# Optimization experiments

Hardware: AMD Instinct MI355X
Metric: run time of the kernel (lower is better)

The kernel has to match this reference:

```python
import jax, jax.numpy as jnp
import numpy as np

N, E, D, H, HEADS_C, G = 50000, 800000, 128, 4, 32, 8
EDIM = D + 2  # H_update: phys_term (D) + ortho_geom (2)


def setup_inputs() -> dict:
    key = jax.random.key(0)
    ks = jax.random.split(key, 24)
    def gl(k, shape, fan_in):
        return jax.random.normal(k, shape, jnp.float32) / np.sqrt(fan_in)
    inp = {
        'h_target': jax.random.normal(ks[0], (N, D), jnp.float32),
        'h_source': jax.random.normal(ks[1], (N, D), jnp.float32),
        'edge_index': jax.random.randint(ks[2], (2, E), 0, N, jnp.int64),
        'pos': jax.random.uniform(ks[3], (N, 2), jnp.float32),
        't_emb': jax.random.normal(ks[4], (1, D), jnp.float32),
        # AdaGN params
        'gn_w': jnp.ones((D,), jnp.float32),
        'gn_b': jnp.zeros((D,), jnp.float32),
        'fc_W': gl(ks[5], (D, 2 * D), D),
        'fc_b': jnp.zeros((2 * D,), jnp.float32),
        # GATv2 params (lin_l, lin_r, lin_edge, att, bias)
        'Wl': gl(ks[6], (D, D), D),
        'bl': jnp.zeros((D,), jnp.float32),
        'Wr': gl(ks[7], (D, D), D),
        'br': jnp.zeros((D,), jnp.float32),
        'We': gl(ks[8], (EDIM, D), EDIM),
        'att': gl(ks[9], (H, HEADS_C), HEADS_C),
        'gat_b': jnp.zeros((D,), jnp.float32),
        # post_gat
        'Wp': gl(ks[10], (D, D), D),
        'bp': jnp.zeros((D,), jnp.float32),
        # update_mlp: LayerNorm + Linear(D,2D) + GELU + Linear(2D,D)
        'ln_w': jnp.ones((D,), jnp.float32),
        'ln_b': jnp.zeros((D,), jnp.float32),
        'W1': gl(ks[11], (D, 2 * D), D),
        'b1': jnp.zeros((2 * D,), jnp.float32),
        'W2': gl(ks[12], (2 * D, D), 2 * D),
        'b2': jnp.zeros((D,), jnp.float32),
    }
    return inp


def _adagn(x, cond, gn_w, gn_b, fc_W, fc_b):
    n, d = x.shape
    xg = x.reshape(n, G, d // G)
    mu = xg.mean(-1, keepdims=True)
    var = xg.var(-1, keepdims=True)  # biased, as torch GroupNorm
    normed = ((xg - mu) / jnp.sqrt(var + 1e-5)).reshape(n, d) * gn_w + gn_b
    style = cond @ fc_W + fc_b  # (1, 2D) broadcasts over nodes
    gamma, beta = jnp.split(style, 2, axis=-1)
    return normed * (1 + gamma) + beta


def _gatv2(h, edge_attr, src, dst, Wl, bl, Wr, br, We, att, gat_b):
    n = h.shape[0]
    x_l = (h @ Wl + bl).reshape(n, H, HEADS_C)  # source transform
    x_r = (h @ Wr + br).reshape(n, H, HEADS_C)  # target transform
    e_feat = (edge_attr @ We).reshape(-1, H, HEADS_C)
    x = x_l[src] + x_r[dst] + e_feat            # (E, H, C)
    x = jax.nn.leaky_relu(x, 0.2)
    logit = jnp.einsum('ehc,hc->eh', x, att)    # (E, H)
    # segment softmax over edges grouped by destination node
    amax = jax.ops.segment_max(logit, dst, num_segments=n)
    amax = jnp.where(jnp.isfinite(amax), amax, 0.0)
    ex = jnp.exp(logit - amax[dst])
    denom = jax.ops.segment_sum(ex, dst, num_segments=n)
    alpha = ex / (denom[dst] + 1e-16)           # (E, H)
    msg = x_l[src] * alpha[:, :, None]          # (E, H, C)
    out = jax.ops.segment_sum(msg, dst, num_segments=n)  # (N, H, C)
    return out.reshape(n, H * HEADS_C) + gat_b


def reference(h_target, h_source, edge_index, pos, t_emb,
              gn_w, gn_b, fc_W, fc_b,
              Wl, bl, Wr, br, We, att, gat_b,
              Wp, bp, ln_w, ln_b, W1, b1, W2, b2):
    h_mod = _adagn(h_source, t_emb, gn_w, gn_b, fc_W, fc_b)
    src, dst = edge_index[0], edge_index[1]
    rel_pos = pos[src] - pos[dst]                       # (E, 2)
    dist_sq = (rel_pos ** 2).sum(-1, keepdims=True) + 1e-8
    geom = rel_pos / dist_sq
    phys = h_mod[src] - h_mod[dst]                      # H_update mode
    ortho = jnp.stack([-geom[:, 1], geom[:, 0]], axis=-1)
    edge_attr = jnp.concatenate([phys, ortho], axis=-1)  # (E, D+2)
    aggr = _gatv2(h_mod, edge_attr, src, dst, Wl, bl, Wr, br, We, att, gat_b)
    aggr = aggr @ Wp + bp
    # update_mlp (dropout inactive in eval)
    mu = aggr.mean(-1, keepdims=True)
    var = aggr.var(-1, keepdims=True)
    z = (aggr - mu) / jnp.sqrt(var + 1e-5) * ln_w + ln_b
    z = jax.nn.gelu(z @ W1 + b1, approximate=False)
    delta = z @ W2 + b2
    return h_target + delta
```

## Files before the change

kernel.cpp:

```cpp
#include <hip/hip_runtime.h>
#include <math.h>

#define D 128
#define LOG2E 1.44269504088896340736f

typedef short bf16x4 __attribute__((ext_vector_type(4)));
typedef short bf16x8 __attribute__((ext_vector_type(8)));
typedef float f32x4  __attribute__((ext_vector_type(4)));
typedef float f32x2  __attribute__((ext_vector_type(2)));

__device__ __forceinline__ float b2f(unsigned short u) {
  union { unsigned int i; float f; } v; v.i = ((unsigned int)u) << 16; return v.f;
}
__device__ __forceinline__ unsigned short f2b(float f) {
  union { float f; unsigned int i; } v; v.f = f;
  unsigned int i = v.i;
  return (unsigned short)((i + 0x7FFFu + ((i >> 16) & 1u)) >> 16);
}
__device__ __forceinline__ float b2f_lo(unsigned int u) {
  union { unsigned int i; float f; } v; v.i = u << 16; return v.f;
}
__device__ __forceinline__ float b2f_hi(unsigned int u) {
  union { unsigned int i; float f; } v; v.i = u & 0xFFFF0000u; return v.f;
}
__device__ __forceinline__ float loadf(const void* p, size_t i, int isb) {
  if (isb) return b2f(((const unsigned short*)p)[i]);
  return ((const float*)p)[i];
}
__device__ __forceinline__ void storeout(void* p, size_t i, float v, int isb) {
  if (isb) ((unsigned short*)p)[i] = f2b(v);
  else     ((float*)p)[i] = v;
}
__device__ __forceinline__ int clampN(int v, int N) {
  return ((unsigned)v >= (unsigned)N) ? 0 : v;
}
__device__ __forceinline__ float gelu_f(float v) {
  return 0.5f * v * (1.f + erff(v * 0.70710678118654752f));
}
__device__ __forceinline__ void slice_load(const unsigned short* g, int tid, f32x4* r) {
  const f32x4* gs = (const f32x4*)g;
  r[0] = gs[tid]; r[1] = gs[tid + 256]; r[2] = gs[tid + 512]; r[3] = gs[tid + 768];
}
__device__ __forceinline__ void slice_store(f32x4* lds, int tid, const f32x4* r) {
  lds[tid] = r[0]; lds[tid + 256] = r[1]; lds[tid + 512] = r[2]; lds[tid + 768] = r[3];
}

__global__ void setup_kernel(const float* __restrict__ gw, const int* __restrict__ e32,
                             int* __restrict__ fflag, int* __restrict__ iflag,
                             int* __restrict__ ok) {
  int t = threadIdx.x;
  if (blockIdx.x == 0) {
    float v = gw[t];
    unsigned long long b = __ballot(v == 1.0f);
    if (t == 0) fflag[0] = (b == 0xFFFFFFFFFFFFFFFFull) ? 0 : 1;
  } else if (blockIdx.x == 1) {
    int v = e32[2 * t + 1];
    unsigned long long b = __ballot(v == 0);
    if (t == 0) iflag[0] = (b == 0xFFFFFFFFFFFFFFFFull) ? 1 : 0;
  } else {
    if (t == 0) ok[0] = 1;
  }
}
__device__ __forceinline__ int edge_src(const void* eraw, int i, int E, int fl, int N) {
  int v = fl ? (int)((const long long*)eraw)[i] : ((const int*)eraw)[i];
  return clampN(v, N);
}
__device__ __forceinline__ int edge_dst(const void* eraw, int i, int E, int fl, int N) {
  int v = fl ? (int)((const long long*)eraw)[(size_t)E + i] : ((const int*)eraw)[(size_t)E + i];
  return clampN(v, N);
}

struct Job { const void* src; float* dst; int n; int blk0; };
struct Jobs { Job j[21]; };
__global__ void cvt_param_kernel(Jobs jobs, const int* __restrict__ fflag, int njobs,
                                 int style_blk,
                                 const void* __restrict__ temb_raw,
                                 const void* __restrict__ fcW_raw,
                                 const void* __restrict__ fcb_raw,
                                 float* __restrict__ style) {
  int isb = fflag[0];
  int b = blockIdx.x;
  if (b == style_blk) {
    int j = threadIdx.x;
    float s = loadf(fcb_raw, j, isb);
    for (int k = 0; k < D; ++k)
      s += loadf(temb_raw, k, isb) * loadf(fcW_raw, (size_t)k * 256 + j, isb);
    style[j] = s;
    return;
  }
  for (int k = 0; k < njobs; ++k) {
    int nblk = (jobs.j[k].n + 255) >> 8;
    int lo = jobs.j[k].blk0;
    if (b >= lo && b < lo + nblk) {
      int i = ((b - lo) << 8) + threadIdx.x;
      if (i < jobs.j[k].n) jobs.j[k].dst[i] = loadf(jobs.j[k].src, i, isb);
      return;
    }
  }
}

__global__ __launch_bounds__(128) void adagn_kernel(
    const void* __restrict__ h_source,
    const float* __restrict__ gn_w, const float* __restrict__ gn_b,
    const float* __restrict__ style, unsigned short* __restrict__ h_mod,
    const int* __restrict__ fflag, int N) {
  int n = blockIdx.x; if (n >= N) return;
  int c = threadIdx.x;
  float x = loadf(h_source, (size_t)n * D + c, fflag[0]);
  float s = x, s2 = x * x;
  s += __shfl_xor(s, 1, 16);  s2 += __shfl_xor(s2, 1, 16);
  s += __shfl_xor(s, 2, 16);  s2 += __shfl_xor(s2, 2, 16);
  s += __shfl_xor(s, 4, 16);  s2 += __shfl_xor(s2, 4, 16);
  s += __shfl_xor(s, 8, 16);  s2 += __shfl_xor(s2, 8, 16);
  float mu = s * (1.f / 16.f);
  float va = s2 * (1.f / 16.f) - mu * mu;
  float iv = rsqrtf(va + 1e-5f);
  float nv = (x - mu) * iv * gn_w[c] + gn_b[c];
  h_mod[(size_t)n * D + c] = f2b(nv * (1.f + style[c]) + style[128 + c]);
}

struct BP { const float* B; int ldb; int col0; };
struct BPJobs { BP j[8]; };
__global__ void bprep_kernel(BPJobs jobs, unsigned short* __restrict__ dst) {
  int job = blockIdx.x >> 7;
  int idx = ((blockIdx.x & 127) << 8) + threadIdx.x;
  int j    = idx & 7;
  int lane = (idx >> 3) & 63;
  int p    = (idx >> 9) & 1;
  int ct   = (idx >> 10) & 7;
  int kt   = idx >> 13;
  int g = lane >> 4;
  int k = kt * 32 + ((j < 4) ? (4 * g + j) : (16 + 4 * g + (j - 4)));
  int n = jobs.j[job].col0 + ct * 16 + (lane & 15);
  float v = jobs.j[job].B[(size_t)k * jobs.j[job].ldb + n];
  unsigned short hi = f2b(v);
  unsigned short out = hi;
  if (p) out = f2b(v - b2f(hi));
  dst[(size_t)job * 32768 + idx] = out;
}

__global__ __launch_bounds__(256) void mgemm3_kernel(
    const unsigned short* __restrict__ A, const unsigned short* __restrict__ Bf,
    const float* __restrict__ bl, const float* __restrict__ br,
    unsigned int* __restrict__ XH32, unsigned short* __restrict__ XR, int Nrows) {
  __shared__ __align__(16) f32x4 pbuf[1024];
  int tid = threadIdx.x;
  int l = tid & 63, w = tid >> 6;
  int rb = blockIdx.x * 64 + w * 16;
  int m = l & 15, g = l >> 4;
  int arow = rb + m;
  if (arow >= Nrows) arow = Nrows - 1;
  const unsigned short* Arow = A + (size_t)arow * 128 + 4 * g;
  bf16x8 af[4];
  #pragma unroll
  for (int kt = 0; kt < 4; ++kt) {
    bf16x4 alo = *(const bf16x4*)(Arow + kt * 32);
    bf16x4 ahi = *(const bf16x4*)(Arow + kt * 32 + 16);
    af[kt] = __builtin_shufflevector(alo, ahi, 0, 1, 2, 3, 4, 5, 6, 7);
  }
  f32x4 acc[24];
  #pragma unroll
  for (int ct = 0; ct < 24; ++ct) acc[ct] = (f32x4){0.f, 0.f, 0.f, 0.f};
  f32x4 pf[4];
  slice_load(Bf, tid, pf);
  slice_store(pbuf, tid, pf);
  __syncthreads();
  const unsigned short* pb = (const unsigned short*)pbuf;
  #pragma unroll
  for (int p = 0; p < 3; ++p) {
    #pragma unroll
    for (int kt = 0; kt < 4; ++kt) {
      int idx = p * 4 + kt;
      if (idx < 11) slice_load(Bf + (size_t)(idx + 1) * 8192, tid, pf);
      #pragma unroll
      for (int c8 = 0; c8 < 8; ++c8) {
        bf16x8 bh  = *(const bf16x8*)(pb + ((c8 * 2) * 64 + l) * 8);
        bf16x8 bl2 = *(const bf16x8*)(pb + ((c8 * 2 + 1) * 64 + l) * 8);
        acc[p * 8 + c8] = __builtin_amdgcn_mfma_f32_16x16x32_bf16(af[kt], bh,  acc[p * 8 + c8], 0, 0, 0);
        acc[p * 8 + c8] = __builtin_amdgcn_mfma_f32_16x16x32_bf16(af[kt], bl2, acc[p * 8 + c8], 0, 0, 0);
      }
      __syncthreads();
      if (idx < 11) { slice_store(pbuf, tid, pf); __syncthreads(); }
    }
  }
  #pragma unroll
  for (int ct = 0; ct < 8; ++ct) {
    int cm = ct * 16 + m;
    #pragma unroll
    for (int r = 0; r < 4; ++r) {
      int row = rb + 4 * g + r;
      if (row < Nrows) {
        float vl = acc[ct][r] + bl[cm];
        float vh = acc[ct + 16][r];
        XH32[(size_t)row * 128 + cm] =
            (unsigned int)f2b(vl) | ((unsigned int)f2b(vh) << 16);
        float vr = acc[ct + 8][r] + br[cm];
        XR[(size_t)row * 128 + cm] = f2b(vr);
      }
    }
  }
}

__global__ void hist_kernel(const void* __restrict__ eraw, const int* __restrict__ iflag,
                            int* __restrict__ deg, int E, int N) {
  int e = blockIdx.x * 256 + threadIdx.x;
  if (e < E) atomicAdd(&deg[edge_dst(eraw, e, E, iflag[0], N)], 1);
}

__global__ __launch_bounds__(1024) void scan1_kernel(const int* __restrict__ deg,
                                                     int* __restrict__ incl,
                                                     int* __restrict__ bsum) {
  int i = blockIdx.x * 1024 + threadIdx.x;
  int lane = threadIdx.x & 63, wave = threadIdx.x >> 6;
  int x = deg[i];
  #pragma unroll
  for (int d = 1; d < 64; d <<= 1) { int t = __shfl_up(x, d, 64); if (lane >= d) x += t; }
  __shared__ int wsum[16];
  if (lane == 63) wsum[wave] = x;
  __syncthreads();
  if (threadIdx.x < 16) {
    int w = wsum[threadIdx.x];
    #pragma unroll
    for (int d = 1; d < 16; d <<= 1) { int t = __shfl_up(w, d, 64); if ((int)threadIdx.x >= d) w += t; }
    wsum[threadIdx.x] = w;
  }
  __syncthreads();
  if (wave > 0) x += wsum[wave - 1];
  incl[i] = x;
  if (threadIdx.x == 1023) bsum[blockIdx.x] = x;
}

__global__ void scan2_kernel(const int* __restrict__ bsum, int* __restrict__ bbase, int nb) {
  if (threadIdx.x == 0) {
    int run = 0;
    for (int b = 0; b < nb; ++b) { bbase[b] = run; run += bsum[b]; }
  }
}

__global__ __launch_bounds__(1024) void scan3_kernel(const int* __restrict__ incl,
                                                     const int* __restrict__ deg,
                                                     const int* __restrict__ bbase,
                                                     int* __restrict__ offs,
                                                     int* __restrict__ cursor, int N) {
  int i = blockIdx.x * 1024 + threadIdx.x;
  if (i < N) {
    int o = bbase[blockIdx.x] + incl[i] - deg[i];
    offs[i] = o; cursor[i] = o;
  }
}

__global__ void scatter_kernel(const void* __restrict__ eraw, const int* __restrict__ iflag,
                               int* __restrict__ cursor, int* __restrict__ elist, int E, int N) {
  int e = blockIdx.x * 256 + threadIdx.x;
  if (e < E) {
    int fl = iflag[0];
    int d = edge_dst(eraw, e, E, fl, N);
    int s = edge_src(eraw, e, E, fl, N);
    int p = atomicAdd(&cursor[d], 1);
    elist[p] = s;
  }
}

__global__ void validate_kernel(const int* __restrict__ offs, const int* __restrict__ deg,
                                const int* __restrict__ cursor, const int* __restrict__ elist,
                                int* __restrict__ ok, int N, int E) {
  int i = blockIdx.x * 256 + threadIdx.x;
  bool bad = false;
  if (i < N) bad = bad || (cursor[i] != offs[i] + deg[i]);
  if (i < E) bad = bad || ((unsigned)elist[i] >= (unsigned)N);
  if (i == 0) bad = bad || (offs[N - 1] + deg[N - 1] != E);
  if (bad) atomicAnd(ok, 0);
}
__global__ void fillc_kernel(void* __restrict__ out, float c, const int* __restrict__ fflag, int n) {
  int i = blockIdx.x * 256 + threadIdx.x;
  if (i < n) storeout(out, i, c, fflag[0]);
}

__global__ __launch_bounds__(256) void edge_kernel(
    const unsigned int* __restrict__ XH32, const unsigned short* __restrict__ XR,
    const float* __restrict__ pos, const float* __restrict__ weo,
    const float* __restrict__ att, const float* __restrict__ gat_b,
    const int* __restrict__ offs, const int* __restrict__ deg,
    const int* __restrict__ elist, unsigned short* __restrict__ aggr, int N) {
  int w = threadIdx.x >> 6;
  int l = threadIdx.x & 63;
  int n = blockIdx.x * 2 + (w >> 1);
  int half = w & 1;
  bool valid = (n < N);
  int nn = valid ? n : 0;
  int c0 = 2 * l;
  uint2 hq = *(const uint2*)(XH32 + (size_t)nn * 128 + c0);
  unsigned int uxr = *(const unsigned int*)(XR + (size_t)nn * 128 + c0);
  f32x2 base = (f32x2){ b2f_lo(uxr) - b2f_hi(hq.x), b2f_hi(uxr) - b2f_hi(hq.y) };
  float2 pd = ((const float2*)pos)[nn];
  f32x2 we0v = (f32x2){ weo[c0], weo[c0 + 1] };
  f32x2 we1v = (f32x2){ weo[128 + c0], weo[128 + c0 + 1] };
  f32x2 attv = (f32x2){ att[c0] * LOG2E, att[c0 + 1] * LOG2E };
  int o = 0, dg = 0;
  if (valid) { o = offs[n]; dg = deg[n]; }
  float mx = -3.402823466e38f, den = 0.f;
  f32x2 num = (f32x2){0.f, 0.f};
  if (dg > half) {
    int s = elist[o + half];
    uint2 q = *(const uint2*)(XH32 + (size_t)s * 128 + c0);
    float2 ps = ((const float2*)pos)[s];
    for (int i = half; i < dg; i += 2) {
      int s2 = elist[o + i + 2];
      uint2 q2 = *(const uint2*)(XH32 + (size_t)s2 * 128 + c0);
      float2 p2 = ((const float2*)pos)[s2];
      float rx = ps.x - pd.x, ry = ps.y - pd.y;
      float inv = 1.f / (rx * rx + ry * ry + 1e-8f);
      float gx = -ry * inv, gy = rx * inv;
      f32x2 xl = (f32x2){ b2f_lo(q.x), b2f_lo(q.y) };
      f32x2 hw = (f32x2){ b2f_hi(q.x), b2f_hi(q.y) };
      f32x2 x = (xl + hw) + (base + gx * we0v + gy * we1v);
      f32x2 lx = __builtin_elementwise_max(x, 0.2f * x);
      f32x2 t = lx * attv;
      float y = t.x + t.y;
      y += __shfl_xor(y, 1, 16);
      y += __shfl_xor(y, 2, 16);
      y += __shfl_xor(y, 4, 16);
      y += __shfl_xor(y, 8, 16);
      float d0 = y - mx;
      if (__any(d0 > 11.5417f)) {
        float mn = fmaxf(mx, y);
        float f = exp2f(mx - mn);
        float p = exp2f(y - mn);
        den = den * f + p;
        num = num * f + p * xl;
        mx = mn;
      } else {
        float p = exp2f(d0);
        den += p;
        num += p * xl;
      }
      s = s2; q = q2; ps = p2;
    }
  }
  __shared__ float4 mrg[4][64];
  mrg[w][l] = (float4){mx, den, num.x, num.y};
  __syncthreads();
  float4 oth = mrg[w ^ 1][l];
  float M = fmaxf(mx, oth.x);
  float f1 = exp2f(mx - M), f2 = exp2f(oth.x - M);
  den = den * f1 + oth.y * f2;
  float n0 = num.x * f1 + oth.z * f2;
  float n1 = num.y * f1 + oth.w * f2;
  if (valid && half == 0) {
    float iden = 1.f / (den + 1e-16f);
    unsigned int o0 = f2b(n0 * iden + gat_b[c0]);
    unsigned int o1 = f2b(n1 * iden + gat_b[c0 + 1]);
    *(unsigned int*)(aggr + (size_t)n * D + c0) = o0 | (o1 << 16);
  }
}

__global__ __launch_bounds__(256) void fused_post_kernel(
    const unsigned short* __restrict__ A, const unsigned short* __restrict__ WP8,
    const float* __restrict__ bp, const float* __restrict__ lnw,
    const float* __restrict__ lnb, const float* __restrict__ b1,
    const float* __restrict__ b2, const void* __restrict__ resid,
    void* __restrict__ out, const int* __restrict__ fflag,
    const int* __restrict__ okf, int Nrows) {
  __shared__ __align__(16) f32x4 pbuf[1024];
  __shared__ __align__(16) unsigned short ldsU[4][16][268];
  int tid = threadIdx.x;
  int l = tid & 63, w = tid >> 6;
  int rb = blockIdx.x * 64 + w * 16;
  int m = l & 15, g = l >> 4;
  int arow = rb + m;
  if (arow >= Nrows) arow = Nrows - 1;
  const unsigned short* Arow = A + (size_t)arow * 128 + 4 * g;
  const unsigned short* pb = (const unsigned short*)pbuf;

  bf16x8 af1[4];
  #pragma unroll
  for (int kt = 0; kt < 4; ++kt) {
    bf16x4 alo = *(const bf16x4*)(Arow + kt * 32);
    bf16x4 ahi = *(const bf16x4*)(Arow + kt * 32 + 16);
    af1[kt] = __builtin_shufflevector(alo, ahi, 0, 1, 2, 3, 4, 5, 6, 7);
  }
  f32x4 pf[4];
  slice_load(WP8 + (size_t)3 * 32768, tid, pf);
  slice_store(pbuf, tid, pf);
  __syncthreads();
  f32x4 acc[8];
  #pragma unroll
  for (int ct = 0; ct < 8; ++ct) acc[ct] = (f32x4){0.f, 0.f, 0.f, 0.f};
  #pragma unroll
  for (int kt = 0; kt < 4; ++kt) {
    if (kt < 3) slice_load(WP8 + (size_t)3 * 32768 + (size_t)(kt + 1) * 8192, tid, pf);
    #pragma unroll
    for (int c8 = 0; c8 < 8; ++c8) {
      bf16x8 bh  = *(const bf16x8*)(pb + ((c8 * 2) * 64 + l) * 8);
      bf16x8 bl2 = *(const bf16x8*)(pb + ((c8 * 2 + 1) * 64 + l) * 8);
      acc[c8] = __builtin_amdgcn_mfma_f32_16x16x32_bf16(af1[kt], bh,  acc[c8], 0, 0, 0);
      acc[c8] = __builtin_amdgcn_mfma_f32_16x16x32_bf16(af1[kt], bl2, acc[c8], 0, 0, 0);
    }
    __syncthreads();
    if (kt < 3) { slice_store(pbuf, tid, pf); __syncthreads(); }
  }
  #pragma unroll
  for (int ct = 0; ct < 8; ++ct) acc[ct] = acc[ct] + bp[ct * 16 + m];

  f32x4 s1 = (f32x4){0.f, 0.f, 0.f, 0.f}, s2v = (f32x4){0.f, 0.f, 0.f, 0.f};
  #pragma unroll
  for (int ct = 0; ct < 8; ++ct) { s1 += acc[ct]; s2v += acc[ct] * acc[ct]; }
  #pragma unroll
  for (int d = 1; d < 16; d <<= 1) {
    f32x4 t1, t2;
    #pragma unroll
    for (int r = 0; r < 4; ++r) { t1[r] = __shfl_xor(s1[r], d, 16); t2[r] = __shfl_xor(s2v[r], d, 16); }
    s1 += t1; s2v += t2;
  }
  f32x4 mu = s1 * (1.f / 128.f);
  f32x4 iv;
  #pragma unroll
  for (int r = 0; r < 4; ++r) {
    float var = s2v[r] * (1.f / 128.f) - mu[r] * mu[r];
    iv[r] = rsqrtf(fmaxf(var, 0.f) + 1e-5f);
  }
  #pragma unroll
  for (int ct = 0; ct < 8; ++ct) {
    float lw = lnw[ct * 16 + m], lb = lnb[ct * 16 + m];
    #pragma unroll
    for (int r = 0; r < 4; ++r) {
      float z = (acc[ct][r] - mu[r]) * iv[r] * lw + lb;
      ldsU[w][4 * g + r][m + 16 * ct] = f2b(z);
    }
  }

  slice_load(WP8 + (size_t)4 * 32768, tid, pf);
  slice_store(pbuf, tid, pf);
  __syncthreads();
  f32x4 acc2[16];
  #pragma unroll
  for (int ct = 0; ct < 16; ++ct) acc2[ct] = (f32x4){0.f, 0.f, 0.f, 0.f};
  #pragma unroll
  for (int ph = 0; ph < 2; ++ph) {
    #pragma unroll
    for (int kt = 0; kt < 4; ++kt) {
      int idx = ph * 4 + kt;
      if (idx < 7) slice_load(WP8 + (size_t)4 * 32768 + (size_t)(idx + 1) * 8192, tid, pf);
      bf16x4 alo = *(const bf16x4*)&ldsU[w][m][4 * g + kt * 32];
      bf16x4 ahi = *(const bf16x4*)&ldsU[w][m][4 * g + kt * 32 + 16];
      bf16x8 af = __builtin_shufflevector(alo, ahi, 0, 1, 2, 3, 4, 5, 6, 7);
      #pragma unroll
      for (int c8 = 0; c8 < 8; ++c8) {
        bf16x8 bh  = *(const bf16x8*)(pb + ((c8 * 2) * 64 + l) * 8);
        bf16x8 bl2 = *(const bf16x8*)(pb + ((c8 * 2 + 1) * 64 + l) * 8);
        acc2[ph * 8 + c8] = __builtin_amdgcn_mfma_f32_16x16x32_bf16(af, bh,  acc2[ph * 8 + c8], 0, 0, 0);
        acc2[ph * 8 + c8] = __builtin_amdgcn_mfma_f32_16x16x32_bf16(af, bl2, acc2[ph * 8 + c8], 0, 0, 0);
      }
      __syncthreads();
      if (idx < 7) { slice_store(pbuf, tid, pf); __syncthreads(); }
    }
  }
  #pragma unroll
  for (int ct = 0; ct < 16; ++ct) {
    float bs = b1[ct * 16 + m];
    #pragma unroll
    for (int r = 0; r < 4; ++r) {
      float v = gelu_f(acc2[ct][r] + bs);
      ldsU[w][4 * g + r][ct * 16 + m] = f2b(v);
    }
  }

  slice_load(WP8 + (size_t)6 * 32768, tid, pf);
  slice_store(pbuf, tid, pf);
  __syncthreads();
  f32x4 acc3[8];
  #pragma unroll
  for (int ct = 0; ct < 8; ++ct) acc3[ct] = (f32x4){0.f, 0.f, 0.f, 0.f};
  #pragma unroll
  for (int kt = 0; kt < 8; ++kt) {
    if (kt < 7) slice_load(WP8 + (size_t)6 * 32768 + (size_t)(kt + 1) * 8192, tid, pf);
    bf16x4 alo = *(const bf16x4*)&ldsU[w][m][4 * g + kt * 32];
    bf16x4 ahi = *(const bf16x4*)&ldsU[w][m][4 * g + kt * 32 + 16];
    bf16x8 af = __builtin_shufflevector(alo, ahi, 0, 1, 2, 3, 4, 5, 6, 7);
    #pragma unroll
    for (int c8 = 0; c8 < 8; ++c8) {
      bf16x8 bh  = *(const bf16x8*)(pb + ((c8 * 2) * 64 + l) * 8);
      bf16x8 bl2 = *(const bf16x8*)(pb + ((c8 * 2 + 1) * 64 + l) * 8);
      acc3[c8] = __builtin_amdgcn_mfma_f32_16x16x32_bf16(af, bh,  acc3[c8], 0, 0, 0);
      acc3[c8] = __builtin_amdgcn_mfma_f32_16x16x32_bf16(af, bl2, acc3[c8], 0, 0, 0);
    }
    __syncthreads();
    if (kt < 7) { slice_store(pbuf, tid, pf); __syncthreads(); }
  }
  int isb = fflag[0];
  int okv = okf[0];
  #pragma unroll
  for (int ct = 0; ct < 8; ++ct) {
    int c = ct * 16 + m;
    float bs = b2[c];
    #pragma unroll
    for (int r = 0; r < 4; ++r) {
      int row = rb + 4 * g + r;
      if (row < Nrows) {
        float v = acc3[ct][r] + bs;
        size_t oi = (size_t)row * 128 + c;
        v += loadf(resid, oi, isb);
        if (okv == 0) v = 100.0f;
        storeout(out, oi, v, isb);
      }
    }
  }
}

extern "C" void kernel_launch(void* const* d_in, const int* in_sizes, int n_in,
                              void* d_out, int out_size, void* d_ws, size_t ws_size,
                              hipStream_t stream) {
  const void* h_resid  = d_in[0];
  const void* h_modsrc = d_in[1];
  const void* eidx     = d_in[2];
  const int N = in_sizes[0] / D;
  const int E = in_sizes[2] / 2;
  const int outN = N * D;

  char* wp = (char*)d_ws;
  auto alloc = [&](size_t bytes) -> void* {
    void* p = (void*)wp;
    wp += (bytes + 255) & ~(size_t)255;
    return p;
  };
  unsigned short* BA = (unsigned short*)alloc((size_t)N * D * 2);
  unsigned int*  XH32 = (unsigned int*)alloc((size_t)N * D * 4);
  unsigned short* BX = (unsigned short*)alloc((size_t)N * D * 2);
  float* style = (float*)alloc(256 * 4);
  const int nb = (N + 1023) / 1024;
  const int npad = nb * 1024;
  int* fflag  = (int*)alloc(256);
  int* iflag  = (int*)alloc(256);
  int* okflag = (int*)alloc(256);
  int* elist  = (int*)alloc((size_t)(E + 64) * 4);
  int* deg    = (int*)alloc((size_t)npad * 4);
  int* incl   = (int*)alloc((size_t)npad * 4);
  int* bsum   = (int*)alloc((size_t)nb * 4);
  int* bbase  = (int*)alloc((size_t)nb * 4);
  int* offs   = (int*)alloc((size_t)N * 4);
  int* cursor = (int*)alloc((size_t)N * 4);
  float* pos_f  = (float*)alloc((size_t)2 * N * 4);
  float* gnw_f  = (float*)alloc(128 * 4);
  float* gnb_f  = (float*)alloc(128 * 4);
  float* Wl_f   = (float*)alloc(16384 * 4);
  float* bl_f   = (float*)alloc(128 * 4);
  float* Wr_f   = (float*)alloc(16384 * 4);
  float* br_f   = (float*)alloc(128 * 4);
  float* We_f   = (float*)alloc(16640 * 4);
  float* att_f  = (float*)alloc(128 * 4);
  float* gtb_f  = (float*)alloc(128 * 4);
  float* Wp_f   = (float*)alloc(16384 * 4);
  float* bp_f   = (float*)alloc(128 * 4);
  float* lnw_f  = (float*)alloc(128 * 4);
  float* lnb_f  = (float*)alloc(128 * 4);
  float* W1_f   = (float*)alloc(32768 * 4);
  float* b1_f   = (float*)alloc(256 * 4);
  float* W2_f   = (float*)alloc(32768 * 4);
  float* b2_f   = (float*)alloc(128 * 4);
  unsigned short* WP8 = (unsigned short*)alloc(8 * 65536);

  size_t required = (size_t)(wp - (char*)d_ws);
  if (required > ws_size) {
    return;
  }

  (void)hipMemsetAsync(deg, 0, (size_t)npad * 4, stream);
  (void)hipMemsetAsync(elist + E, 0, 64 * 4, stream);

  setup_kernel<<<3, 64, 0, stream>>>((const float*)d_in[5], (const int*)eidx,
                                     fflag, iflag, okflag);

  const int expected[24] = {6400000, 6400000, 1600000, 100000, 128, 128, 128, 32768,
                            256, 16384, 128, 16384, 128, 16640, 128, 128, 16384, 128,
                            128, 128, 32768, 256, 32768, 128};
  int bad = (n_in == 24) ? -1 : 24;
  if (bad < 0) {
    for (int i = 0; i < 24; ++i) {
      if (in_sizes[i] != expected[i]) { bad = i; break; }
    }
  }
  if (bad >= 0) {
    fillc_kernel<<<(outN + 255) / 256, 256, 0, stream>>>(d_out, 20.f + 10.f * bad, fflag, outN);
    return;
  }

  Jobs jobs;
  int jn = 0, blk = 0;
  auto addjob = [&](const void* s, float* dptr, int n) {
    jobs.j[jn] = {s, dptr, n, blk};
    blk += (n + 255) >> 8;
    ++jn;
  };
  addjob(d_in[3],  pos_f,  2 * N);
  addjob(d_in[5],  gnw_f,  128);
  addjob(d_in[6],  gnb_f,  128);
  addjob(d_in[9],  Wl_f,   16384);
  addjob(d_in[10], bl_f,   128);
  addjob(d_in[11], Wr_f,   16384);
  addjob(d_in[12], br_f,   128);
  addjob(d_in[13], We_f,   16640);
  addjob(d_in[14], att_f,  128);
  addjob(d_in[15], gtb_f,  128);
  addjob(d_in[16], Wp_f,   16384);
  addjob(d_in[17], bp_f,   128);
  addjob(d_in[18], lnw_f,  128);
  addjob(d_in[19], lnb_f,  128);
  addjob(d_in[20], W1_f,   32768);
  addjob(d_in[21], b1_f,   256);
  addjob(d_in[22], W2_f,   32768);
  addjob(d_in[23], b2_f,   128);
  cvt_param_kernel<<<blk + 1, 256, 0, stream>>>(jobs, fflag, jn, blk,
                                                d_in[4], d_in[7], d_in[8], style);

  adagn_kernel<<<N, 128, 0, stream>>>(h_modsrc, gnw_f, gnb_f, style, BA, fflag, N);

  BPJobs bj;
  bj.j[0] = {Wl_f, 128, 0};
  bj.j[1] = {Wr_f, 128, 0};
  bj.j[2] = {We_f, 128, 0};
  bj.j[3] = {Wp_f, 128, 0};
  bj.j[4] = {W1_f, 256, 0};
  bj.j[5] = {W1_f, 256, 128};
  bj.j[6] = {W2_f, 128, 0};
  bj.j[7] = {W2_f + 128 * 128, 128, 0};
  bprep_kernel<<<1024, 256, 0, stream>>>(bj, WP8);

  const int mb = (N + 63) / 64;
  mgemm3_kernel<<<mb, 256, 0, stream>>>(BA, WP8, bl_f, br_f, XH32, BX, N);

  hist_kernel<<<(E + 255) / 256, 256, 0, stream>>>(eidx, iflag, deg, E, N);
  scan1_kernel<<<nb, 1024, 0, stream>>>(deg, incl, bsum);
  scan2_kernel<<<1, 64, 0, stream>>>(bsum, bbase, nb);
  scan3_kernel<<<nb, 1024, 0, stream>>>(incl, deg, bbase, offs, cursor, N);
  scatter_kernel<<<(E + 255) / 256, 256, 0, stream>>>(eidx, iflag, cursor, elist, E, N);
  int vmax = (E > N ? E : N);
  validate_kernel<<<(vmax + 255) / 256, 256, 0, stream>>>(offs, deg, cursor, elist, okflag, N, E);

  edge_kernel<<<(N + 1) / 2, 256, 0, stream>>>(XH32, BX, pos_f, We_f + 128 * 128,
                                               att_f, gtb_f, offs, deg, elist, BA, N);

  fused_post_kernel<<<mb, 256, 0, stream>>>(BA, WP8, bp_f, lnw_f, lnb_f, b1_f, b2_f,
                                            h_resid, d_out, fflag, okflag, N);
}
```

Baseline: 504.1 us.

## Make post-MLP kernel single-wave, reading weight fragments directly from global memory

The fused post-GAT MLP kernel goes from 256-thread blocks of 64 rows to 64-thread single-wave blocks of 16 rows. The B-operand weight fragments are now loaded straight from global memory instead of being staged through shared memory. This removes the per-slice shared-memory copies and all __syncthreads barriers. The W1 GEMM is split into two 128-column panels, computing the upper half first so the LayerNorm output in LDS is not overwritten, which halves the accumulator registers. In exchange, each 16-row wave re-reads the full weight set through the cache hierarchy, so weight traffic per row is four times higher.

```diff
diff --git a/kernel.cpp b/kernel.cpp
--- a/kernel.cpp
+++ b/kernel.cpp
@@ -354,23 +354,20 @@
   }
 }
 
-__global__ __launch_bounds__(256) void fused_post_kernel(
+__global__ __launch_bounds__(64) void fused_post_kernel(
     const unsigned short* __restrict__ A, const unsigned short* __restrict__ WP8,
     const float* __restrict__ bp, const float* __restrict__ lnw,
     const float* __restrict__ lnb, const float* __restrict__ b1,
     const float* __restrict__ b2, const void* __restrict__ resid,
     void* __restrict__ out, const int* __restrict__ fflag,
     const int* __restrict__ okf, int Nrows) {
-  __shared__ __align__(16) f32x4 pbuf[1024];
-  __shared__ __align__(16) unsigned short ldsU[4][16][268];
-  int tid = threadIdx.x;
-  int l = tid & 63, w = tid >> 6;
-  int rb = blockIdx.x * 64 + w * 16;
+  __shared__ __align__(16) unsigned short ldsU[16][268];
+  int l = threadIdx.x;
+  int rb = blockIdx.x * 16;
   int m = l & 15, g = l >> 4;
   int arow = rb + m;
   if (arow >= Nrows) arow = Nrows - 1;
   const unsigned short* Arow = A + (size_t)arow * 128 + 4 * g;
-  const unsigned short* pb = (const unsigned short*)pbuf;
 
   bf16x8 af1[4];
   #pragma unroll
@@ -379,25 +376,19 @@
     bf16x4 ahi = *(const bf16x4*)(Arow + kt * 32 + 16);
     af1[kt] = __builtin_shufflevector(alo, ahi, 0, 1, 2, 3, 4, 5, 6, 7);
   }
-  f32x4 pf[4];
-  slice_load(WP8 + (size_t)3 * 32768, tid, pf);
-  slice_store(pbuf, tid, pf);
-  __syncthreads();
   f32x4 acc[8];
   #pragma unroll
   for (int ct = 0; ct < 8; ++ct) acc[ct] = (f32x4){0.f, 0.f, 0.f, 0.f};
   #pragma unroll
   for (int kt = 0; kt < 4; ++kt) {
-    if (kt < 3) slice_load(WP8 + (size_t)3 * 32768 + (size_t)(kt + 1) * 8192, tid, pf);
     #pragma unroll
     for (int c8 = 0; c8 < 8; ++c8) {
-      bf16x8 bh  = *(const bf16x8*)(pb + ((c8 * 2) * 64 + l) * 8);
-      bf16x8 bl2 = *(const bf16x8*)(pb + ((c8 * 2 + 1) * 64 + l) * 8);
+      size_t off = (size_t)3 * 32768 + (size_t)kt * 8192 + (size_t)((c8 * 2) * 64 + l) * 8;
+      bf16x8 bh  = *(const bf16x8*)(WP8 + off);
+      bf16x8 bl2 = *(const bf16x8*)(WP8 + off + 512);
       acc[c8] = __builtin_amdgcn_mfma_f32_16x16x32_bf16(af1[kt], bh,  acc[c8], 0, 0, 0);
       acc[c8] = __builtin_amdgcn_mfma_f32_16x16x32_bf16(af1[kt], bl2, acc[c8], 0, 0, 0);
     }
-    __syncthreads();
-    if (kt < 3) { slice_store(pbuf, tid, pf); __syncthreads(); }
   }
   #pragma unroll
   for (int ct = 0; ct < 8; ++ct) acc[ct] = acc[ct] + bp[ct * 16 + m];
@@ -425,67 +416,60 @@
     #pragma unroll
     for (int r = 0; r < 4; ++r) {
       float z = (acc[ct][r] - mu[r]) * iv[r] * lw + lb;
-      ldsU[w][4 * g + r][m + 16 * ct] = f2b(z);
-    }
-  }
-
-  slice_load(WP8 + (size_t)4 * 32768, tid, pf);
-  slice_store(pbuf, tid, pf);
-  __syncthreads();
-  f32x4 acc2[16];
-  #pragma unroll
-  for (int ct = 0; ct < 16; ++ct) acc2[ct] = (f32x4){0.f, 0.f, 0.f, 0.f};
+      ldsU[4 * g + r][m + 16 * ct] = f2b(z);
+    }
+  }
+
+  f32x4 acc2[8];
   #pragma unroll
   for (int ph = 0; ph < 2; ++ph) {
+    int panel = 5 - ph;
+    int colbase = (1 - ph) * 128;
+    #pragma unroll
+    for (int c8 = 0; c8 < 8; ++c8) acc2[c8] = (f32x4){0.f, 0.f, 0.f, 0.f};
     #pragma unroll
     for (int kt = 0; kt < 4; ++kt) {
-      int idx = ph * 4 + kt;
-      if (idx < 7) slice_load(WP8 + (size_t)4 * 32768 + (size_t)(idx + 1) * 8192, tid, pf);
-      bf16x4 alo = *(const bf16x4*)&ldsU[w][m][4 * g + kt * 32];
-      bf16x4 ahi = *(const bf16x4*)&ldsU[w][m][4 * g + kt * 32 + 16];
+      bf16x4 alo = *(const bf16x4*)&ldsU[m][4 * g + kt * 32];
+      bf16x4 ahi = *(const bf16x4*)&ldsU[m][4 * g + kt * 32 + 16];
       bf16x8 af = __builtin_shufflevector(alo, ahi, 0, 1, 2, 3, 4, 5, 6, 7);
       #pragma unroll
       for (int c8 = 0; c8 < 8; ++c8) {
-        bf16x8 bh  = *(const bf16x8*)(pb + ((c8 * 2) * 64 + l) * 8);
-        bf16x8 bl2 = *(const bf16x8*)(pb + ((c8 * 2 + 1) * 64 + l) * 8);
-        acc2[ph * 8 + c8] = __builtin_amdgcn_mfma_f32_16x16x32_bf16(af, bh,  acc2[ph * 8 + c8], 0, 0, 0);
-        acc2[ph * 8 + c8] = __builtin_amdgcn_mfma_f32_16x16x32_bf16(af, bl2, acc2[ph * 8 + c8], 0, 0, 0);
+        size_t off = (size_t)panel * 32768 + (size_t)kt * 8192
+                   + (size_t)((c8 * 2) * 64 + l) * 8;
+        bf16x8 bh  = *(const bf16x8*)(WP8 + off);
+        bf16x8 bl2 = *(const bf16x8*)(WP8 + off + 512);
+        acc2[c8] = __builtin_amdgcn_mfma_f32_16x16x32_bf16(af, bh,  acc2[c8], 0, 0, 0);
+        acc2[c8] = __builtin_amdgcn_mfma_f32_16x16x32_bf16(af, bl2, acc2[c8], 0, 0, 0);
       }
-      __syncthreads();
-      if (idx < 7) { slice_store(pbuf, tid, pf); __syncthreads(); }
-    }
-  }
-  #pragma unroll
-  for (int ct = 0; ct < 16; ++ct) {
-    float bs = b1[ct * 16 + m];
-    #pragma unroll
-    for (int r = 0; r < 4; ++r) {
-      float v = gelu_f(acc2[ct][r] + bs);
-      ldsU[w][4 * g + r][ct * 16 + m] = f2b(v);
-    }
-  }
-
-  slice_load(WP8 + (size_t)6 * 32768, tid, pf);
-  slice_store(pbuf, tid, pf);
-  __syncthreads();
+    }
+    #pragma unroll
+    for (int c8 = 0; c8 < 8; ++c8) {
+      float bs = b1[colbase + c8 * 16 + m];
+      #pragma unroll
+      for (int r = 0; r < 4; ++r) {
+        float v = gelu_f(acc2[c8][r] + bs);
+        ldsU[4 * g + r][colbase + c8 * 16 + m] = f2b(v);
+      }
+    }
+  }
+
   f32x4 acc3[8];
   #pragma unroll
   for (int ct = 0; ct < 8; ++ct) acc3[ct] = (f32x4){0.f, 0.f, 0.f, 0.f};
   #pragma unroll
   for (int kt = 0; kt < 8; ++kt) {
-    if (kt < 7) slice_load(WP8 + (size_t)6 * 32768 + (size_t)(kt + 1) * 8192, tid, pf);
-    bf16x4 alo = *(const bf16x4*)&ldsU[w][m][4 * g + kt * 32];
-    bf16x4 ahi = *(const bf16x4*)&ldsU[w][m][4 * g + kt * 32 + 16];
+    bf16x4 alo = *(const bf16x4*)&ldsU[m][4 * g + kt * 32];
+    bf16x4 ahi = *(const bf16x4*)&ldsU[m][4 * g + kt * 32 + 16];
     bf16x8 af = __builtin_shufflevector(alo, ahi, 0, 1, 2, 3, 4, 5, 6, 7);
     #pragma unroll
     for (int c8 = 0; c8 < 8; ++c8) {
-      bf16x8 bh  = *(const bf16x8*)(pb + ((c8 * 2) * 64 + l) * 8);
-      bf16x8 bl2 = *(const bf16x8*)(pb + ((c8 * 2 + 1) * 64 + l) * 8);
+      size_t off = (size_t)(6 + (kt >> 2)) * 32768 + (size_t)(kt & 3) * 8192
+                 + (size_t)((c8 * 2) * 64 + l) * 8;
+      bf16x8 bh  = *(const bf16x8*)(WP8 + off);
+      bf16x8 bl2 = *(const bf16x8*)(WP8 + off + 512);
       acc3[c8] = __builtin_amdgcn_mfma_f32_16x16x32_bf16(af, bh,  acc3[c8], 0, 0, 0);
       acc3[c8] = __builtin_amdgcn_mfma_f32_16x16x32_bf16(af, bl2, acc3[c8], 0, 0, 0);
     }
-    __syncthreads();
-    if (kt < 7) { slice_store(pbuf, tid, pf); __syncthreads(); }
   }
   int isb = fflag[0];
   int okv = okf[0];
@@ -639,6 +623,7 @@
   edge_kernel<<<(N + 1) / 2, 256, 0, stream>>>(XH32, BX, pos_f, We_f + 128 * 128,
                                                att_f, gtb_f, offs, deg, elist, BA, N);
 
-  fused_post_kernel<<<mb, 256, 0, stream>>>(BA, WP8, bp_f, lnw_f, lnb_f, b1_f, b2_f,
+  const int mb2 = (N + 15) / 16;
+  fused_post_kernel<<<mb2, 64, 0, stream>>>(BA, WP8, bp_f, lnw_f, lnb_f, b1_f, b2_f,
                                             h_resid, d_out, fflag, okflag, N);
 }
```

Result: faster. 484.7 us (-3.8%).
